# Kernel optimization log

Hardware: AMD Instinct MI355X
Metric: run time of the kernel (lower is better)

Reference implementation:

```python
import jax, jax.numpy as jnp
import numpy as np
from jax import lax

LATENT_DIM = 512
TOKEN_DIM = 256
KERNEL = 5
STRIDE = 5


def setup_inputs() -> dict:
    key = jax.random.key(0)
    ks = jax.random.split(key, 8)
    B, L, S = 8, 1024, 10240
    s = lambda fan_in: 1.0 / np.sqrt(fan_in)
    return {
        "latents": jax.random.normal(ks[0], (B, L, LATENT_DIM), dtype=jnp.float32),
        "tokens": jax.random.normal(ks[1], (B, S, TOKEN_DIM), dtype=jnp.float32),
        # nn.Linear weights, stored as (out, in) like torch
        "W_lat": jax.random.uniform(ks[2], (LATENT_DIM, LATENT_DIM), jnp.float32, -s(LATENT_DIM), s(LATENT_DIM)),
        "W_tok": jax.random.uniform(ks[3], (LATENT_DIM, LATENT_DIM), jnp.float32, -s(LATENT_DIM), s(LATENT_DIM)),
        "W_vlat": jax.random.uniform(ks[4], (LATENT_DIM, LATENT_DIM), jnp.float32, -s(LATENT_DIM), s(LATENT_DIM)),
        "W_vtok": jax.random.uniform(ks[5], (LATENT_DIM, LATENT_DIM), jnp.float32, -s(LATENT_DIM), s(LATENT_DIM)),
        # Conv1d weight (out_ch, in_ch, k) and bias
        "conv_w": jax.random.uniform(ks[6], (LATENT_DIM, TOKEN_DIM, KERNEL), jnp.float32, -s(TOKEN_DIM * KERNEL), s(TOKEN_DIM * KERNEL)),
        "conv_b": jax.random.uniform(ks[7], (LATENT_DIM,), jnp.float32, -s(TOKEN_DIM * KERNEL), s(TOKEN_DIM * KERNEL)),
    }


def reference(latents, tokens, W_lat, W_tok, W_vlat, W_vtok, conv_w, conv_b):
    # Conv1d: (B,S,token_dim) -> (B,S//5,latent_dim)
    tok = lax.conv_general_dilated(
        tokens.transpose(0, 2, 1), conv_w, window_strides=(STRIDE,),
        padding="VALID", dimension_numbers=("NCH", "OIH", "NCH"))
    tok = (tok + conv_b[None, :, None]).transpose(0, 2, 1)  # (B, S', D)

    R_lat = jnp.einsum("bld,ed->ble", latents, W_lat)
    R_tok = jnp.einsum("bsd,ed->bse", tok, W_tok)
    V_lat = jnp.einsum("bld,ed->ble", latents, W_vlat)
    V_tok = jnp.einsum("bsd,ed->bse", tok, W_vtok)

    # shared score matrix, used for both row-wise and column-wise softmax
    A = jnp.einsum("ble,bse->bls", R_lat, R_tok) / jnp.sqrt(jnp.float32(LATENT_DIM))
    delta_lat = jnp.einsum("bls,bse->ble", jax.nn.softmax(A, axis=-1), V_tok)
    delta_tok = jnp.einsum("bls,ble->bse", jax.nn.softmax(A, axis=1), V_lat)

    updated_latents = latents + delta_lat
    updated_tokens = tok + delta_tok
    output = jnp.concatenate([updated_latents, updated_tokens], axis=1)
    return (updated_latents, updated_tokens, output)
```

## Files before the change

kernel.cpp:

```cpp
#include <hip/hip_runtime.h>
#include <math.h>

#define SCALEF 0.044194173824159216f

typedef __attribute__((ext_vector_type(8))) short bf16x8;
typedef __attribute__((ext_vector_type(4))) float f32x4;

static __device__ __forceinline__ unsigned short f2bf(float f) {
    union { float f; unsigned int i; } v; v.f = f;
    return (unsigned short)((v.i + 0x7fffu + ((v.i >> 16) & 1u)) >> 16);
}
static __device__ __forceinline__ float bf2f(unsigned short h) {
    union { unsigned int i; float f; } v; v.i = ((unsigned int)h) << 16;
    return v.f;
}
static __device__ __forceinline__ void gload16(const void* g, void* l) {
    __builtin_amdgcn_global_load_lds(
        (const __attribute__((address_space(1))) unsigned int*)g,
        (__attribute__((address_space(3))) unsigned int*)l, 16, 0, 0);
}
static __device__ __forceinline__ int swz(int l, int n) {
    return (l & 7) * (n >> 3) + (l >> 3);
}

__global__ __launch_bounds__(256) void cvt_tl(const float4* __restrict__ tok,
                                              const float4* __restrict__ lat,
                                              ushort4* __restrict__ tokd,
                                              ushort4* __restrict__ latd) {
    long t = blockIdx.x * 256L + threadIdx.x;
    #pragma unroll
    for (int k = 0; k < 5; ++k) {
        long i = t + k * 1048576L;
        float4 f = tok[i];
        ushort4 u; u.x = f2bf(f.x); u.y = f2bf(f.y); u.z = f2bf(f.z); u.w = f2bf(f.w);
        tokd[i] = u;
    }
    {
        float4 f = lat[t];
        ushort4 u; u.x = f2bf(f.x); u.y = f2bf(f.y); u.z = f2bf(f.z); u.w = f2bf(f.w);
        latd[t] = u;
    }
}

__global__ __launch_bounds__(256) void prep_rest(
    const float* __restrict__ wl, const float* __restrict__ wt,
    const float4* __restrict__ wvl, const float4* __restrict__ wvt,
    const float* __restrict__ cw,
    ushort4* __restrict__ wlT, ushort4* __restrict__ wtT,
    ushort4* __restrict__ wvlb, ushort4* __restrict__ wvtb,
    unsigned int* __restrict__ wpb)
{
    const long NW = 65536, NCV = 327680;
    for (long i = blockIdx.x * 256L + threadIdx.x; i < 4 * NW + NCV;
         i += gridDim.x * 256L) {
        long r = i;
        if (r < 2 * NW) {
            const float* src = (r < NW) ? wl : wt;
            ushort4* dst = (r < NW) ? wlT : wtT;
            long u = (r < NW) ? r : r - NW;
            int a = (int)(u >> 7), e4 = (int)(u & 127);
            ushort4 o;
            o.x = f2bf(src[(e4 * 4 + 0) * 512 + a]);
            o.y = f2bf(src[(e4 * 4 + 1) * 512 + a]);
            o.z = f2bf(src[(e4 * 4 + 2) * 512 + a]);
            o.w = f2bf(src[(e4 * 4 + 3) * 512 + a]);
            dst[a * 128 + e4] = o;
            continue;
        }
        r -= 2 * NW;
        const float4* s; ushort4* d;
        if (r < NW) { s = wvl; d = wvlb; }
        else if ((r -= NW) < NW) { s = wvt; d = wvtb; }
        else {
            r -= NW;
            long e = r / 640, rr = r % 640, k = rr >> 7, c2 = rr & 127;
            unsigned int lo = f2bf(cw[e * 1280 + (2 * c2) * 5 + k]);
            unsigned int hi = f2bf(cw[e * 1280 + (2 * c2 + 1) * 5 + k]);
            wpb[r] = lo | (hi << 16);
            continue;
        }
        float4 f = s[r];
        ushort4 u; u.x = f2bf(f.x); u.y = f2bf(f.y); u.z = f2bf(f.z); u.w = f2bf(f.w);
        d[r] = u;
    }
}

template<int RL>
static __device__ __forceinline__ void sm_body(unsigned short* __restrict__ rowp,
                                               float* __restrict__ redm,
                                               float* __restrict__ reds) {
    constexpr int U = RL / 512;
    unsigned int* p = (unsigned int*)rowp;
    const int t = threadIdx.x, lane = t & 63, wid = t >> 6;
    unsigned int u[U];
    float v[2 * U];
    #pragma unroll
    for (int i = 0; i < U; ++i) u[i] = p[t + (i << 8)];
    #pragma unroll
    for (int i = 0; i < U; ++i) {
        v[2 * i]     = bf2f((unsigned short)(u[i] & 0xffffu));
        v[2 * i + 1] = bf2f((unsigned short)(u[i] >> 16));
    }
    float m = -INFINITY;
    #pragma unroll
    for (int i = 0; i < 2 * U; ++i) m = fmaxf(m, v[i]);
    #pragma unroll
    for (int k = 1; k < 64; k <<= 1) m = fmaxf(m, __shfl_xor(m, k));
    if (lane == 0) redm[wid] = m;
    __syncthreads();
    m = fmaxf(fmaxf(redm[0], redm[1]), fmaxf(redm[2], redm[3]));
    float s = 0.f, e[2 * U];
    #pragma unroll
    for (int i = 0; i < 2 * U; ++i) { e[i] = __expf(v[i] - m); s += e[i]; }
    #pragma unroll
    for (int k = 1; k < 64; k <<= 1) s += __shfl_xor(s, k);
    if (lane == 0) reds[wid] = s;
    __syncthreads();
    s = reds[0] + reds[1] + reds[2] + reds[3];
    float inv = 1.f / s;
    #pragma unroll
    for (int i = 0; i < U; ++i) {
        unsigned int lo = f2bf(e[2 * i] * inv);
        unsigned int hi = f2bf(e[2 * i + 1] * inv);
        p[t + (i << 8)] = lo | (hi << 16);
    }
}

__global__ __launch_bounds__(256) void softmax_both(unsigned short* __restrict__ S,
                                                    unsigned short* __restrict__ ST) {
    __shared__ float redm[4], reds[4];
    long b = blockIdx.x;
    if (b < 8192) sm_body<2048>(S + b * 2048L, redm, reds);
    else          sm_body<1024>(ST + (b - 8192) * 1024L, redm, reds);
}

template<int AMODE, int EPI>
static __device__ __forceinline__ void mm_body(
    char* __restrict__ smc, int bx, int by, int z,
    const unsigned short* __restrict__ A, const unsigned short* __restrict__ B,
    long bsA, long bsB, int lda, int ldb, int K,
    unsigned short* __restrict__ Cb, long bsCb,
    float* __restrict__ C0, long bsC0, float* __restrict__ C1, long bsC1,
    const void* __restrict__ basep, long bsBase, int ldc, float scale)
{
    const int t = threadIdx.x, lane = t & 63, wid = t >> 6;
    const int m0 = by << 7, n0 = bx << 7;
    const unsigned short* Ab = A + (long)z * bsA;
    const unsigned short* Bb = B + (long)z * bsB;

    const int rA0 = wid * 16 + (lane >> 2);
    const int rA1 = rA0 + 64;
    const int cs0 = (lane & 3) ^ ((rA0 >> 1) & 3);
    const int cs1 = (lane & 3) ^ ((rA1 >> 1) & 3);

    long aoff0, aoff1;
    if (AMODE == 0) {
        aoff0 = (long)(m0 + rA0) * lda + cs0 * 8;
        aoff1 = (long)(m0 + rA1) * lda + cs1 * 8;
    } else {
        int ma = m0 + rA0, mb = m0 + rA1;
        aoff0 = (long)(ma >> 11) * 2621440 + (long)(ma & 2047) * 1280 + cs0 * 8;
        aoff1 = (long)(mb >> 11) * 2621440 + (long)(mb & 2047) * 1280 + cs1 * 8;
    }
    const long boff0 = (long)(n0 + rA0) * ldb + cs0 * 8;
    const long boff1 = (long)(n0 + rA1) * ldb + cs1 * 8;

    const int dA0 = (wid << 10), dA1 = ((wid + 4) << 10);
    const int dB0 = 8192 + (wid << 10), dB1 = 8192 + ((wid + 4) << 10);

    const int wr = wid >> 1, wc = wid & 1;
    const int l15 = lane & 15, cslot = lane >> 4;
    int offA[4], offB[4];
    #pragma unroll
    for (int i = 0; i < 4; ++i) {
        int r = wr * 64 + i * 16 + l15;
        offA[i] = r * 64 + ((cslot ^ ((r >> 1) & 3)) << 4);
        int rb = wc * 64 + i * 16 + l15;
        offB[i] = 8192 + rb * 64 + ((cslot ^ ((rb >> 1) & 3)) << 4);
    }

    f32x4 acc[4][4];
    #pragma unroll
    for (int i = 0; i < 4; ++i)
        #pragma unroll
        for (int j = 0; j < 4; ++j)
            acc[i][j] = (f32x4)(0.f);

#define STAGE(p, ktv) do {                                   \
        int kb_ = (ktv);                                     \
        int bo_ = (p) * 16384;                               \
        gload16(Ab + aoff0 + kb_, smc + bo_ + dA0);          \
        gload16(Ab + aoff1 + kb_, smc + bo_ + dA1);          \
        gload16(Bb + boff0 + kb_, smc + bo_ + dB0);          \
        gload16(Bb + boff1 + kb_, smc + bo_ + dB1);          \
    } while (0)

    const int nt = K >> 5;
    STAGE(0, 0);
    STAGE(1, 32);
    int cur = 0;
    for (int it = 0; it < nt; ++it) {
        if (it + 2 < nt) {
            int nx2 = (cur >= 1) ? cur - 1 : 2;
            STAGE(nx2, (it + 2) << 5);
            asm volatile("s_waitcnt vmcnt(8)" ::: "memory");
        } else if (it + 1 < nt) {
            asm volatile("s_waitcnt vmcnt(4)" ::: "memory");
        } else {
            asm volatile("s_waitcnt vmcnt(0)" ::: "memory");
        }
        __builtin_amdgcn_s_barrier();
        const char* base = smc + cur * 16384;
        bf16x8 af[4], bfr[4];
        #pragma unroll
        for (int i = 0; i < 4; ++i) af[i]  = *(const bf16x8*)(base + offA[i]);
        #pragma unroll
        for (int i = 0; i < 4; ++i) bfr[i] = *(const bf16x8*)(base + offB[i]);
        #pragma unroll
        for (int i = 0; i < 4; ++i)
            #pragma unroll
            for (int j = 0; j < 4; ++j)
                acc[i][j] = __builtin_amdgcn_mfma_f32_16x16x32_bf16(af[i], bfr[j], acc[i][j], 0, 0, 0);
        asm volatile("s_waitcnt lgkmcnt(0)" ::: "memory");
        __builtin_amdgcn_s_barrier();
        cur = (cur + 1 == 3) ? 0 : cur + 1;
    }
#undef STAGE

    const int colb = n0 + wc * 64 + l15;
    const int rowb = m0 + wr * 64 + cslot * 4;
    if (EPI == 4) {
        unsigned short* STp = (unsigned short*)C0;
        #pragma unroll
        for (int i = 0; i < 4; ++i) {
            #pragma unroll
            for (int j = 0; j < 4; ++j) {
                int n = colb + j * 16;
                int mb = rowb + i * 16;
                float v0 = acc[i][j][0] * scale, v1 = acc[i][j][1] * scale;
                float v2 = acc[i][j][2] * scale, v3 = acc[i][j][3] * scale;
                unsigned short b0 = f2bf(v0), b1 = f2bf(v1), b2 = f2bf(v2), b3 = f2bf(v3);
                unsigned short* sp = Cb + (long)z * bsCb + (long)mb * ldc + n;
                sp[0] = b0; sp[ldc] = b1; sp[2 * ldc] = b2; sp[3 * ldc] = b3;
                ushort4 st4; st4.x = b0; st4.y = b1; st4.z = b2; st4.w = b3;
                *(ushort4*)(STp + (long)z * bsC0 + (long)n * bsC1 + mb) = st4;
            }
        }
        return;
    }
    #pragma unroll
    for (int i = 0; i < 4; ++i) {
        #pragma unroll
        for (int j = 0; j < 4; ++j) {
            int n = colb + j * 16;
            #pragma unroll
            for (int q = 0; q < 4; ++q) {
                int m = rowb + i * 16 + q;
                float v = acc[i][j][q];
                if (EPI == 0) {
                    Cb[(long)z * bsCb + (long)m * ldc + n] = f2bf(v * scale);
                } else if (EPI == 1) {
                    v += ((const float*)basep)[n];
                    Cb[(long)m * ldc + n] = f2bf(v);
                } else if (EPI == 2) {
                    float bv = ((const float*)basep)[(long)z * bsBase + (long)m * ldc + n];
                    float o = bv + v;
                    C0[(long)z * bsC0 + (long)m * ldc + n] = o;
                    C1[(long)z * bsC1 + (long)m * ldc + n] = o;
                } else {
                    float bv = bf2f(((const unsigned short*)basep)[(long)z * bsBase + (long)m * ldc + n]);
                    float o = bv + v;
                    C0[(long)z * bsC0 + (long)m * ldc + n] = o;
                    C1[(long)z * bsC1 + (long)m * ldc + n] = o;
                }
            }
        }
    }
}

__global__ __launch_bounds__(256) void gemm_g1(
    const unsigned short* __restrict__ tknb, const unsigned short* __restrict__ wpb,
    const float* __restrict__ conv_b, unsigned short* __restrict__ tokb,
    const unsigned short* __restrict__ latb,
    const unsigned short* __restrict__ wvlb, unsigned short* __restrict__ vlT,
    const unsigned short* __restrict__ wtT, const unsigned short* __restrict__ wlT,
    unsigned short* __restrict__ Mt)
{
    __shared__ unsigned short sm[24576];
    char* smc = (char*)sm;
    const int bid = blockIdx.x;
    if (bid < 512) {
        int l = swz(bid, 512);
        mm_body<1, 1>(smc, l & 3, l >> 2, 0, tknb, wpb, 0, 0, 1280, 1280, 1280,
                      tokb, 0, nullptr, 0, nullptr, 0, conv_b, 0, 512, 1.f);
    } else if (bid < 768) {
        int l = swz(bid - 512, 256);
        mm_body<0, 0>(smc, l & 7, (l >> 3) & 3, l >> 5, wvlb, latb, 0, 524288,
                      512, 512, 512, vlT, 524288, nullptr, 0, nullptr, 0,
                      nullptr, 0, 1024, 1.f);
    } else {
        int l = bid - 768;
        mm_body<0, 0>(smc, l & 3, l >> 2, 0, wtT, wlT, 0, 0, 512, 512, 512,
                      Mt, 0, nullptr, 0, nullptr, 0, nullptr, 0, 512, 1.f);
    }
}

__global__ __launch_bounds__(256) void gemm_g2(
    const unsigned short* __restrict__ tokb,
    const unsigned short* __restrict__ wvtb, unsigned short* __restrict__ vtT,
    const unsigned short* __restrict__ latb, const unsigned short* __restrict__ Mt,
    unsigned short* __restrict__ P)
{
    __shared__ unsigned short sm[24576];
    char* smc = (char*)sm;
    const int bid = blockIdx.x;
    if (bid < 512) {
        int l = swz(bid, 512);
        mm_body<0, 0>(smc, l & 15, (l >> 4) & 3, l >> 6, wvtb, tokb, 0, 1048576,
                      512, 512, 512, vtT, 1048576, nullptr, 0, nullptr, 0,
                      nullptr, 0, 2048, 1.f);
    } else {
        int l = swz(bid - 512, 256);
        mm_body<0, 0>(smc, l & 3, l >> 2, 0, latb, Mt, 0, 0, 512, 512, 512,
                      P, 0, nullptr, 0, nullptr, 0, nullptr, 0, 512, 1.f);
    }
}

__global__ __launch_bounds__(256) void gemm_sc(
    const unsigned short* __restrict__ P, const unsigned short* __restrict__ tokb,
    unsigned short* __restrict__ S, unsigned short* __restrict__ ST)
{
    __shared__ unsigned short sm[24576];
    int l = swz((int)blockIdx.x, 1024);
    mm_body<0, 4>((char*)sm, l & 15, (l >> 4) & 7, l >> 7,
                  P, tokb, 524288, 1048576, 512, 512, 512,
                  S, 2097152, (float*)ST, 2097152, nullptr, 1024,
                  nullptr, 0, 2048, SCALEF);
}

__global__ __launch_bounds__(256) void gemm_g3(
    const unsigned short* __restrict__ S, const unsigned short* __restrict__ ST,
    const unsigned short* __restrict__ vlT, const unsigned short* __restrict__ vtT,
    const float* __restrict__ latents, const unsigned short* __restrict__ tokb,
    float* __restrict__ out)
{
    __shared__ unsigned short sm[24576];
    char* smc = (char*)sm;
    const int bid = blockIdx.x;
    if (bid < 256) {
        int l = swz(bid, 256);
        mm_body<0, 2>(smc, l & 3, (l >> 2) & 7, l >> 5, S, vtT, 2097152, 1048576,
                      2048, 2048, 2048, nullptr, 0,
                      out, 524288, out + 12582912, 1572864,
                      latents, 524288, 512, 1.f);
    } else {
        int l = swz(bid - 256, 512);
        mm_body<0, 3>(smc, l & 3, (l >> 2) & 15, l >> 6, ST, vlT, 2097152, 524288,
                      1024, 1024, 1024, nullptr, 0,
                      out + 4194304, 1048576, out + 12582912 + 524288, 1572864,
                      tokb, 1048576, 512, 1.f);
    }
}

extern "C" void kernel_launch(void* const* d_in, const int* in_sizes, int n_in,
                              void* d_out, int out_size, void* d_ws, size_t ws_size,
                              hipStream_t stream)
{
    const float* latents = (const float*)d_in[0];
    const float* tokens  = (const float*)d_in[1];
    const float* W_lat   = (const float*)d_in[2];
    const float* W_tok   = (const float*)d_in[3];
    const float* W_vlat  = (const float*)d_in[4];
    const float* W_vtok  = (const float*)d_in[5];
    const float* conv_w  = (const float*)d_in[6];
    const float* conv_b  = (const float*)d_in[7];
    float* out = (float*)d_out;
    char* ws = (char*)d_ws;

    unsigned short* S    = (unsigned short*)(ws);
    unsigned short* ST   = (unsigned short*)(ws + 33554432);
    unsigned short* tokb = (unsigned short*)(ws + 67108864);
    unsigned short* latb = (unsigned short*)(ws + 83886080);
    unsigned short* P    = (unsigned short*)(ws + 92274688);
    unsigned short* Mt   = (unsigned short*)(ws + 100663296);
    unsigned short* vlT  = (unsigned short*)(ws + 117440512);
    unsigned short* vtT  = (unsigned short*)(ws + 125829120);
    unsigned short* wpb  = (unsigned short*)(ws + 142606336);
    unsigned short* wlT  = (unsigned short*)(ws + 143917056);
    unsigned short* wtT  = (unsigned short*)(ws + 144441344);
    unsigned short* wvlb = (unsigned short*)(ws + 144965632);
    unsigned short* wvtb = (unsigned short*)(ws + 145489920);
    unsigned short* tknb = (unsigned short*)(out + 12582912);

    cvt_tl<<<4096, 256, 0, stream>>>((const float4*)tokens, (const float4*)latents,
                                     (ushort4*)tknb, (ushort4*)latb);
    prep_rest<<<512, 256, 0, stream>>>(
        W_lat, W_tok, (const float4*)W_vlat, (const float4*)W_vtok, conv_w,
        (ushort4*)wlT, (ushort4*)wtT, (ushort4*)wvlb, (ushort4*)wvtb,
        (unsigned int*)wpb);

    gemm_g1<<<784, 256, 0, stream>>>(tknb, wpb, conv_b, tokb,
                                     latb, wvlb, vlT, wtT, wlT, Mt);

    gemm_g2<<<768, 256, 0, stream>>>(tokb, wvtb, vtT, latb, Mt, P);

    gemm_sc<<<1024, 256, 0, stream>>>(P, tokb, S, ST);

    softmax_both<<<24576, 256, 0, stream>>>(S, ST);

    gemm_g3<<<768, 256, 0, stream>>>(S, ST, vlT, vtT, latents, tokb, out);
}
```

Before: 225.5 us.

## Use double-buffered LDS in score GEMM and fold Mt GEMM into conversion kernel

Adds an NBUF template parameter to the shared GEMM body so the score GEMM (gemm_sc) can run with two LDS stages (32KB) instead of three (48KB). The aim is more resident blocks per CU and better latency hiding. The small W_tok^T·W_lat product (Mt) moves from gemm_g1 into the fp32→bf16 conversion kernel, which takes the tail of that grid and shortens gemm_g1. The cost is a shallower prefetch pipeline in gemm_sc, which may expose memory latency.

```diff
diff --git a/kernel.cpp b/kernel.cpp
--- a/kernel.cpp
+++ b/kernel.cpp
@@ -21,25 +21,6 @@
 }
 static __device__ __forceinline__ int swz(int l, int n) {
     return (l & 7) * (n >> 3) + (l >> 3);
-}
-
-__global__ __launch_bounds__(256) void cvt_tl(const float4* __restrict__ tok,
-                                              const float4* __restrict__ lat,
-                                              ushort4* __restrict__ tokd,
-                                              ushort4* __restrict__ latd) {
-    long t = blockIdx.x * 256L + threadIdx.x;
-    #pragma unroll
-    for (int k = 0; k < 5; ++k) {
-        long i = t + k * 1048576L;
-        float4 f = tok[i];
-        ushort4 u; u.x = f2bf(f.x); u.y = f2bf(f.y); u.z = f2bf(f.z); u.w = f2bf(f.w);
-        tokd[i] = u;
-    }
-    {
-        float4 f = lat[t];
-        ushort4 u; u.x = f2bf(f.x); u.y = f2bf(f.y); u.z = f2bf(f.z); u.w = f2bf(f.w);
-        latd[t] = u;
-    }
 }
 
 __global__ __launch_bounds__(256) void prep_rest(
@@ -134,7 +115,7 @@
     else          sm_body<1024>(ST + (b - 8192) * 1024L, redm, reds);
 }
 
-template<int AMODE, int EPI>
+template<int AMODE, int EPI, int NBUF>
 static __device__ __forceinline__ void mm_body(
     char* __restrict__ smc, int bx, int by, int z,
     const unsigned short* __restrict__ A, const unsigned short* __restrict__ B,
@@ -194,38 +175,61 @@
         gload16(Bb + boff0 + kb_, smc + bo_ + dB0);          \
         gload16(Bb + boff1 + kb_, smc + bo_ + dB1);          \
     } while (0)
+#define COMPUTE(c) do {                                                        \
+        const char* base_ = smc + (c) * 16384;                                 \
+        bf16x8 af[4], bfr[4];                                                  \
+        _Pragma("unroll")                                                      \
+        for (int i = 0; i < 4; ++i) af[i]  = *(const bf16x8*)(base_ + offA[i]);\
+        _Pragma("unroll")                                                      \
+        for (int i = 0; i < 4; ++i) bfr[i] = *(const bf16x8*)(base_ + offB[i]);\
+        _Pragma("unroll")                                                      \
+        for (int i = 0; i < 4; ++i)                                            \
+            _Pragma("unroll")                                                  \
+            for (int j = 0; j < 4; ++j)                                        \
+                acc[i][j] = __builtin_amdgcn_mfma_f32_16x16x32_bf16(           \
+                    af[i], bfr[j], acc[i][j], 0, 0, 0);                        \
+    } while (0)
 
     const int nt = K >> 5;
-    STAGE(0, 0);
-    STAGE(1, 32);
-    int cur = 0;
-    for (int it = 0; it < nt; ++it) {
-        if (it + 2 < nt) {
-            int nx2 = (cur >= 1) ? cur - 1 : 2;
-            STAGE(nx2, (it + 2) << 5);
-            asm volatile("s_waitcnt vmcnt(8)" ::: "memory");
-        } else if (it + 1 < nt) {
-            asm volatile("s_waitcnt vmcnt(4)" ::: "memory");
-        } else {
-            asm volatile("s_waitcnt vmcnt(0)" ::: "memory");
-        }
-        __builtin_amdgcn_s_barrier();
-        const char* base = smc + cur * 16384;
-        bf16x8 af[4], bfr[4];
-        #pragma unroll
-        for (int i = 0; i < 4; ++i) af[i]  = *(const bf16x8*)(base + offA[i]);
-        #pragma unroll
-        for (int i = 0; i < 4; ++i) bfr[i] = *(const bf16x8*)(base + offB[i]);
-        #pragma unroll
-        for (int i = 0; i < 4; ++i)
-            #pragma unroll
-            for (int j = 0; j < 4; ++j)
-                acc[i][j] = __builtin_amdgcn_mfma_f32_16x16x32_bf16(af[i], bfr[j], acc[i][j], 0, 0, 0);
-        asm volatile("s_waitcnt lgkmcnt(0)" ::: "memory");
-        __builtin_amdgcn_s_barrier();
-        cur = (cur + 1 == 3) ? 0 : cur + 1;
+    if constexpr (NBUF == 3) {
+        STAGE(0, 0);
+        STAGE(1, 32);
+        int cur = 0;
+        for (int it = 0; it < nt; ++it) {
+            if (it + 2 < nt) {
+                int nx2 = (cur >= 1) ? cur - 1 : 2;
+                STAGE(nx2, (it + 2) << 5);
+                asm volatile("s_waitcnt vmcnt(8)" ::: "memory");
+            } else if (it + 1 < nt) {
+                asm volatile("s_waitcnt vmcnt(4)" ::: "memory");
+            } else {
+                asm volatile("s_waitcnt vmcnt(0)" ::: "memory");
+            }
+            __builtin_amdgcn_s_barrier();
+            COMPUTE(cur);
+            asm volatile("s_waitcnt lgkmcnt(0)" ::: "memory");
+            __builtin_amdgcn_s_barrier();
+            cur = (cur + 1 == 3) ? 0 : cur + 1;
+        }
+    } else {
+        STAGE(0, 0);
+        int cur = 0;
+        for (int it = 0; it < nt; ++it) {
+            if (it + 1 < nt) {
+                STAGE(cur ^ 1, (it + 1) << 5);
+                asm volatile("s_waitcnt vmcnt(4)" ::: "memory");
+            } else {
+                asm volatile("s_waitcnt vmcnt(0)" ::: "memory");
+            }
+            __builtin_amdgcn_s_barrier();
+            COMPUTE(cur);
+            asm volatile("s_waitcnt lgkmcnt(0)" ::: "memory");
+            __builtin_amdgcn_s_barrier();
+            cur ^= 1;
+        }
     }
 #undef STAGE
+#undef COMPUTE
 
     const int colb = n0 + wc * 64 + l15;
     const int rowb = m0 + wr * 64 + cslot * 4;
@@ -278,30 +282,51 @@
     }
 }
 
+__global__ __launch_bounds__(256) void cvt_mt(
+    const float4* __restrict__ tok, const float4* __restrict__ lat,
+    ushort4* __restrict__ tokd, ushort4* __restrict__ latd,
+    const unsigned short* __restrict__ wtT, const unsigned short* __restrict__ wlT,
+    unsigned short* __restrict__ Mt)
+{
+    __shared__ unsigned short sm[16384];
+    const int bid = blockIdx.x;
+    if (bid < 4096) {
+        long t = bid * 256L + threadIdx.x;
+        #pragma unroll
+        for (int k = 0; k < 5; ++k) {
+            long i = t + k * 1048576L;
+            float4 f = tok[i];
+            ushort4 u; u.x = f2bf(f.x); u.y = f2bf(f.y); u.z = f2bf(f.z); u.w = f2bf(f.w);
+            tokd[i] = u;
+        }
+        float4 f = lat[t];
+        ushort4 u; u.x = f2bf(f.x); u.y = f2bf(f.y); u.z = f2bf(f.z); u.w = f2bf(f.w);
+        latd[t] = u;
+    } else {
+        int l = bid - 4096;
+        mm_body<0, 0, 2>((char*)sm, l & 3, l >> 2, 0, wtT, wlT, 0, 0, 512, 512, 512,
+                         Mt, 0, nullptr, 0, nullptr, 0, nullptr, 0, 512, 1.f);
+    }
+}
+
 __global__ __launch_bounds__(256) void gemm_g1(
     const unsigned short* __restrict__ tknb, const unsigned short* __restrict__ wpb,
     const float* __restrict__ conv_b, unsigned short* __restrict__ tokb,
     const unsigned short* __restrict__ latb,
-    const unsigned short* __restrict__ wvlb, unsigned short* __restrict__ vlT,
-    const unsigned short* __restrict__ wtT, const unsigned short* __restrict__ wlT,
-    unsigned short* __restrict__ Mt)
+    const unsigned short* __restrict__ wvlb, unsigned short* __restrict__ vlT)
 {
     __shared__ unsigned short sm[24576];
     char* smc = (char*)sm;
     const int bid = blockIdx.x;
     if (bid < 512) {
         int l = swz(bid, 512);
-        mm_body<1, 1>(smc, l & 3, l >> 2, 0, tknb, wpb, 0, 0, 1280, 1280, 1280,
-                      tokb, 0, nullptr, 0, nullptr, 0, conv_b, 0, 512, 1.f);
-    } else if (bid < 768) {
+        mm_body<1, 1, 3>(smc, l & 3, l >> 2, 0, tknb, wpb, 0, 0, 1280, 1280, 1280,
+                         tokb, 0, nullptr, 0, nullptr, 0, conv_b, 0, 512, 1.f);
+    } else {
         int l = swz(bid - 512, 256);
-        mm_body<0, 0>(smc, l & 7, (l >> 3) & 3, l >> 5, wvlb, latb, 0, 524288,
-                      512, 512, 512, vlT, 524288, nullptr, 0, nullptr, 0,
-                      nullptr, 0, 1024, 1.f);
-    } else {
-        int l = bid - 768;
-        mm_body<0, 0>(smc, l & 3, l >> 2, 0, wtT, wlT, 0, 0, 512, 512, 512,
-                      Mt, 0, nullptr, 0, nullptr, 0, nullptr, 0, 512, 1.f);
+        mm_body<0, 0, 3>(smc, l & 7, (l >> 3) & 3, l >> 5, wvlb, latb, 0, 524288,
+                         512, 512, 512, vlT, 524288, nullptr, 0, nullptr, 0,
+                         nullptr, 0, 1024, 1.f);
     }
 }
 
@@ -316,13 +341,13 @@
     const int bid = blockIdx.x;
     if (bid < 512) {
         int l = swz(bid, 512);
-        mm_body<0, 0>(smc, l & 15, (l >> 4) & 3, l >> 6, wvtb, tokb, 0, 1048576,
-                      512, 512, 512, vtT, 1048576, nullptr, 0, nullptr, 0,
-                      nullptr, 0, 2048, 1.f);
+        mm_body<0, 0, 3>(smc, l & 15, (l >> 4) & 3, l >> 6, wvtb, tokb, 0, 1048576,
+                         512, 512, 512, vtT, 1048576, nullptr, 0, nullptr, 0,
+                         nullptr, 0, 2048, 1.f);
     } else {
         int l = swz(bid - 512, 256);
-        mm_body<0, 0>(smc, l & 3, l >> 2, 0, latb, Mt, 0, 0, 512, 512, 512,
-                      P, 0, nullptr, 0, nullptr, 0, nullptr, 0, 512, 1.f);
+        mm_body<0, 0, 3>(smc, l & 3, l >> 2, 0, latb, Mt, 0, 0, 512, 512, 512,
+                         P, 0, nullptr, 0, nullptr, 0, nullptr, 0, 512, 1.f);
     }
 }
 
@@ -330,12 +355,12 @@
     const unsigned short* __restrict__ P, const unsigned short* __restrict__ tokb,
     unsigned short* __restrict__ S, unsigned short* __restrict__ ST)
 {
-    __shared__ unsigned short sm[24576];
+    __shared__ unsigned short sm[16384];
     int l = swz((int)blockIdx.x, 1024);
-    mm_body<0, 4>((char*)sm, l & 15, (l >> 4) & 7, l >> 7,
-                  P, tokb, 524288, 1048576, 512, 512, 512,
-                  S, 2097152, (float*)ST, 2097152, nullptr, 1024,
-                  nullptr, 0, 2048, SCALEF);
+    mm_body<0, 4, 2>((char*)sm, l & 15, (l >> 4) & 7, l >> 7,
+                     P, tokb, 524288, 1048576, 512, 512, 512,
+                     S, 2097152, (float*)ST, 2097152, nullptr, 1024,
+                     nullptr, 0, 2048, SCALEF);
 }
 
 __global__ __launch_bounds__(256) void gemm_g3(
@@ -349,16 +374,16 @@
     const int bid = blockIdx.x;
     if (bid < 256) {
         int l = swz(bid, 256);
-        mm_body<0, 2>(smc, l & 3, (l >> 2) & 7, l >> 5, S, vtT, 2097152, 1048576,
-                      2048, 2048, 2048, nullptr, 0,
-                      out, 524288, out + 12582912, 1572864,
-                      latents, 524288, 512, 1.f);
+        mm_body<0, 2, 3>(smc, l & 3, (l >> 2) & 7, l >> 5, S, vtT, 2097152, 1048576,
+                         2048, 2048, 2048, nullptr, 0,
+                         out, 524288, out + 12582912, 1572864,
+                         latents, 524288, 512, 1.f);
     } else {
         int l = swz(bid - 256, 512);
-        mm_body<0, 3>(smc, l & 3, (l >> 2) & 15, l >> 6, ST, vlT, 2097152, 524288,
-                      1024, 1024, 1024, nullptr, 0,
-                      out + 4194304, 1048576, out + 12582912 + 524288, 1572864,
-                      tokb, 1048576, 512, 1.f);
+        mm_body<0, 3, 3>(smc, l & 3, (l >> 2) & 15, l >> 6, ST, vlT, 2097152, 524288,
+                         1024, 1024, 1024, nullptr, 0,
+                         out + 4194304, 1048576, out + 12582912 + 524288, 1572864,
+                         tokb, 1048576, 512, 1.f);
     }
 }
 
@@ -392,15 +417,15 @@
     unsigned short* wvtb = (unsigned short*)(ws + 145489920);
     unsigned short* tknb = (unsigned short*)(out + 12582912);
 
-    cvt_tl<<<4096, 256, 0, stream>>>((const float4*)tokens, (const float4*)latents,
-                                     (ushort4*)tknb, (ushort4*)latb);
     prep_rest<<<512, 256, 0, stream>>>(
         W_lat, W_tok, (const float4*)W_vlat, (const float4*)W_vtok, conv_w,
         (ushort4*)wlT, (ushort4*)wtT, (ushort4*)wvlb, (ushort4*)wvtb,
         (unsigned int*)wpb);
 
-    gemm_g1<<<784, 256, 0, stream>>>(tknb, wpb, conv_b, tokb,
-                                     latb, wvlb, vlT, wtT, wlT, Mt);
+    cvt_mt<<<4112, 256, 0, stream>>>((const float4*)tokens, (const float4*)latents,
+                                     (ushort4*)tknb, (ushort4*)latb, wtT, wlT, Mt);
+
+    gemm_g1<<<768, 256, 0, stream>>>(tknb, wpb, conv_b, tokb, latb, wvlb, vlT);
 
     gemm_g2<<<768, 256, 0, stream>>>(tokb, wvtb, vtT, latb, Mt, P);
 
```

New measurement: 226.4 us. No clear change (+0.4%).
